# Kernel optimization log

Hardware: AMD Instinct MI355X
Metric: run time of the kernel (lower is better)

Reference implementation:

```python
import jax, jax.numpy as jnp
from jax import lax
import numpy as np

N_HOS, N_TYPES, N_STRUCTS = 4, 16, 512
N_COMBOS = N_HOS * N_TYPES  # 64
HID = 1024
N_ITERS = 60  # fixed PDHG iterations (differentiable unrolled solver)


def setup_inputs() -> dict:
    key = jax.random.key(0)
    ks = jax.random.split(key, 8)
    X = jax.random.uniform(ks[0], (2048, N_HOS, N_TYPES), dtype=jnp.float32)
    # sparse 0/1 structure matrix; guarantee each structure touches >=1 combo
    S = (jax.random.uniform(ks[1], (N_COMBOS, N_STRUCTS)) < 0.08).astype(jnp.float32)
    cols = jnp.arange(N_STRUCTS)
    S = S.at[cols % N_COMBOS, cols].set(1.0)
    # MLP params (He-ish init)
    W1 = jax.random.normal(ks[2], (N_COMBOS, HID), dtype=jnp.float32) * (2.0 / N_COMBOS) ** 0.5
    b1 = jnp.zeros((HID,), jnp.float32)
    W2 = jax.random.normal(ks[3], (HID, HID), dtype=jnp.float32) * (2.0 / HID) ** 0.5
    b2 = jnp.zeros((HID,), jnp.float32)
    W3 = jax.random.normal(ks[4], (HID, N_STRUCTS), dtype=jnp.float32) * (2.0 / HID) ** 0.5
    b3 = jnp.zeros((N_STRUCTS,), jnp.float32)
    return {"X": X, "W1": W1, "b1": b1, "W2": W2, "b2": b2,
            "W3": W3, "b3": b3, "S": S, "batch_size": 2048}


def nn_forward(X, W1, b1, W2, b2, W3, b3):
    # torch loop applies act_fun after EVERY layer, including the last
    Z = X.reshape(X.shape[0], -1)                 # [B, n_hos*n_types]
    Z = jax.nn.relu(Z @ W1 + b1)
    Z = jax.nn.relu(Z @ W2 + b2)
    Z = jax.nn.relu(Z @ W3 + b3)                  # [B, n_structures]
    return Z


def solve_lp(S, W, B, Z, n_iters=N_ITERS):
    """Batched solve of: max_x W.x - ||x - Z||_2  s.t. x >= 0, S x <= B.
    PDHG (Chambolle-Pock) on  min_x f(x) + i{Kx <= c},
    f(x) = -W.x + ||x - Z||_2,  K = [S; -I],  c = [B; 0].
    Same optimization problem as the CvxpyLayer, solved by a fixed-iteration
    batched primal-dual method (differentiable via unrolling)."""
    batch, n = Z.shape
    m = S.shape[0]

    # ||K||_2 via power iteration on K^T K = S^T S + I (constant wrt params)
    def pow_step(v, _):
        v2 = S.T @ (S @ v) + v
        return v2 / jnp.linalg.norm(v2), None
    v0 = jnp.full((n,), 1.0 / np.sqrt(n), Z.dtype)
    v, _ = lax.scan(pow_step, v0, None, length=30)
    L = jnp.sqrt(jnp.vdot(v, S.T @ (S @ v) + v))
    L = lax.stop_gradient(L)
    tau = 0.9 / L
    sigma = 0.9 / L

    c = jnp.concatenate([B, jnp.zeros_like(Z)], axis=-1)  # [B, m+n]

    def Kx(x):
        return jnp.concatenate([x @ S.T, -x], axis=-1)    # [B, m+n]

    def KTy(y):
        return y[:, :m] @ S - y[:, m:]                    # [B, n]

    def prox_f(v):
        # argmin_x 1/(2 tau) ||x - v||^2 - W.x + ||x - Z||_2
        u = v + tau * W
        d = u - Z
        nrm = jnp.linalg.norm(d, axis=-1, keepdims=True)
        scale = jnp.maximum(1.0 - tau / jnp.maximum(nrm, 1e-12), 0.0)
        return Z + scale * d

    def step(carry, _):
        x, xbar, y = carry
        y = jnp.maximum(y + sigma * (Kx(xbar) - c), 0.0)
        x_new = prox_f(x - tau * KTy(y))
        xbar = 2.0 * x_new - x
        return (x_new, xbar, y), None

    x0 = jnp.zeros_like(Z)
    y0 = jnp.zeros((batch, m + n), Z.dtype)
    (x, _, _), _ = lax.scan(step, (x0, x0, y0), None, length=n_iters)
    return x


def reference(X, W1, b1, W2, b2, W3, b3, S, batch_size):
    Z = nn_forward(X, W1, b1, W2, b2, W3, b3)     # [B, n_structures]
    W = jnp.ones_like(Z)                          # weights w = 1 (as in torch)
    B = X.reshape(batch_size, -1)                 # capacities b
    return solve_lp(S, W, B, Z)
```

## Files before the change

### kernel.cpp

```cpp
#include <hip/hip_runtime.h>


typedef _Float16 half8 __attribute__((ext_vector_type(8)));
typedef __fp16 fp16x2 __attribute__((ext_vector_type(2)));
typedef __fp16 fp16x4 __attribute__((ext_vector_type(4)));
typedef float floatx4 __attribute__((ext_vector_type(4)));

#define BATCH 2048
#define NITERS 60
#define XBS 520
#define YLS 72
#define H1S 1032

template <int CTRL>
__device__ __forceinline__ float dpp_addf(float x) {
    int y = __builtin_amdgcn_update_dpp(0, __builtin_bit_cast(int, x), CTRL, 0xf, 0xf, true);
    return x + __builtin_bit_cast(float, y);
}
__device__ __forceinline__ float sum16(float x) {
    x = dpp_addf<0xB1>(x);
    x = dpp_addf<0x4E>(x);
    x = dpp_addf<0x124>(x);
    x = dpp_addf<0x128>(x);
    return x;
}
__device__ __forceinline__ float sum64(float x) {
    x = sum16(x);
    x += __builtin_bit_cast(float, __builtin_amdgcn_ds_swizzle(__builtin_bit_cast(int, x), 0x401F));
    x += __shfl_xor(x, 32, 64);
    return x;
}

__device__ void power_64(const float* __restrict__ S, float* __restrict__ tau_g) {
    __shared__ unsigned long long rowm[64][8];
    __shared__ float G[64][65];
    __shared__ float wl[64], pg[4][64];
    int t = threadIdx.x, wv = t >> 6, ln = t & 63;
    for (int rr = 0; rr < 16; rr++) {
        int r = wv * 16 + rr;
        float v[8];
#pragma unroll
        for (int e = 0; e < 8; e++) v[e] = S[r * 512 + e * 64 + ln];
#pragma unroll
        for (int e = 0; e < 8; e++) {
            unsigned long long m = __ballot(v[e] != 0.f);
            if (ln == 0) rowm[r][e] = m;
        }
    }
    __syncthreads();
    for (int k = 0; k < 16; k++) {
        int idx = t * 16 + k;
        int i = idx >> 6, j = idx & 63;
        int cnt = 0;
#pragma unroll
        for (int e = 0; e < 8; e++) cnt += __popcll(rowm[i][e] & rowm[j][e]);
        G[i][j] = (float)cnt;
    }
    if (wv == 0) {
        int cnt = 0;
#pragma unroll
        for (int e = 0; e < 8; e++) cnt += __popcll(rowm[ln][e]);
        wl[ln] = (float)cnt * 0.044194173824159216f;
    }
    __syncthreads();
    for (int s = 0; s < 30; s++) {
        float a = 0.f;
#pragma unroll
        for (int jj = 0; jj < 16; jj++) {
            int j = wv * 16 + jj;
            a += G[ln][j] * wl[j];
        }
        pg[wv][ln] = a;
        __syncthreads();
        if (wv == 0) {
            float g = (pg[0][ln] + pg[1][ln]) + (pg[2][ln] + pg[3][ln]);
            float wi = wl[ln];
            float s1 = sum64(wi * g);
            float s2 = sum64(wi * wi);
            float n = sqrtf(s1 + 2.f * s2 + 1.f);
            wl[ln] = (g + wi) / n;
        }
        __syncthreads();
    }
    if (wv == 0) {
        float wi = wl[ln];
        float s2 = sum64(wi * wi);
        if (ln == 0) tau_g[0] = 0.9f / sqrtf(s2 + 1.f);
    }
}

__global__ __launch_bounds__(256) void prep(
    const float* __restrict__ W1, _Float16* __restrict__ w1f,
    const float* __restrict__ W2, _Float16* __restrict__ w2f,
    const float* __restrict__ W3, _Float16* __restrict__ w3f,
    const float* __restrict__ S, _Float16* __restrict__ s1f,
    _Float16* __restrict__ s2f, float* __restrict__ tau_g) {
    int tid = threadIdx.x;
    int bid = blockIdx.x;
    if (bid < 32) {
        int i0 = (bid * 256 + tid) * 8;
        int lane = (i0 >> 3) & 63, cf = (i0 >> 9) & 63, kk = i0 >> 15;
        int col = (cf >> 4) * 256 + (cf & 15) * 16 + (lane & 15);
        int kb = kk * 32 + ((lane >> 4) << 3);
        half8 vv;
#pragma unroll
        for (int j = 0; j < 8; j++)
            vv[j] = (_Float16)W1[(size_t)(kb + j) * 1024 + col];
        *(half8*)&w1f[i0] = vv;
        return;
    }
    if (bid < 544) {
        int i0 = ((bid - 32) * 256 + tid) * 8;
        int lane = (i0 >> 3) & 63, cf = (i0 >> 9) & 63, ks = i0 >> 15;
        int col = (cf >> 4) * 256 + (cf & 15) * 16 + (lane & 15);
        int kb = ks * 32 + ((lane >> 4) << 3);
        half8 vv;
#pragma unroll
        for (int j = 0; j < 8; j++)
            vv[j] = (_Float16)W2[(size_t)(kb + j) * 1024 + col];
        *(half8*)&w2f[i0] = vv;
        return;
    }
    if (bid < 800) {
        int i0 = ((bid - 544) * 256 + tid) * 8;
        int lane = (i0 >> 3) & 63, cf = (i0 >> 9) & 31, ks = i0 >> 14;
        int col = (cf >> 3) * 128 + (cf & 7) * 16 + (lane & 15);
        int kb = ks * 32 + ((lane >> 4) << 3);
        half8 vv;
#pragma unroll
        for (int j = 0; j < 8; j++)
            vv[j] = (_Float16)W3[(size_t)(kb + j) * 512 + col];
        *(half8*)&w3f[i0] = vv;
        return;
    }
    if (bid < 1056) {
        int i = (bid - 800) * 256 + tid;
        if (i < 4 * 16 * 64 * 8) {
            int j = i & 7, lane = (i >> 3) & 63, kk = (i >> 9) & 15, wc = i >> 13;
            int pos = kk * 32 + (lane >> 4) * 8 + j;
            int pp = pos >> 7, r = pos & 127;
            int hh = r >> 6, r2 = r & 63;
            int lmc = r2 >> 2, t3 = r2 & 3;
            int c = pp * 128 + (hh * 4 + t3) * 16 + lmc;
            int m = wc * 16 + (lane & 15);
            s1f[i] = (_Float16)S[m * 512 + c];
        } else {
            int i2 = i - 4 * 16 * 64 * 8;
            int j = i2 & 7, lane = (i2 >> 3) & 63, c = (i2 >> 9) & 1,
                tt = (i2 >> 10) & 7, wc = i2 >> 13;
            int kc = c * 32 + (lane >> 4) * 8 + j;
            int n = wc * 128 + tt * 16 + (lane & 15);
            s2f[i2] = (_Float16)S[kc * 512 + n];
        }
        return;
    }
    power_64(S, tau_g);
}

__global__ __launch_bounds__(256, 1) void mega(
    const float* __restrict__ X,
    const _Float16* __restrict__ w1f, const float* __restrict__ b1,
    const _Float16* __restrict__ w2f, const float* __restrict__ b2,
    const _Float16* __restrict__ w3f, const float* __restrict__ b3,
    const _Float16* __restrict__ s1f, const _Float16* __restrict__ s2f,
    const float* __restrict__ tau_p, float* __restrict__ out) {
    __shared__ __align__(16) char smem[34304];
    _Float16* H1 = (_Float16*)smem;
    _Float16* H2 = (_Float16*)(smem + 16512);
    _Float16* X8 = (_Float16*)(smem + 33024);
    _Float16* xb_d = (_Float16*)smem;
    _Float16* yl_d = (_Float16*)(smem + 8320);
    float (*red)[4] = (float(*)[4])(smem + 9472);

    int tid = threadIdx.x;
    int wp = tid >> 6;
    int l = tid & 63, lm = l & 15, q = l >> 4;
    int lq = lm & 7;
    int qa = q & 1, h = q >> 1;
    int b0 = blockIdx.x * 8;

    if (tid < 128) {
        int r = tid >> 4, c = (tid & 15) * 4;
        floatx4 v = *(const floatx4*)&X[(size_t)(b0 + r) * 64 + c];
        fp16x4 hh = {(__fp16)v.x, (__fp16)v.y, (__fp16)v.z, (__fp16)v.w};
        *(fp16x4*)&X8[r * 72 + c] = hh;
    }
    __syncthreads();

    {
        floatx4 acc1[16] = {};
#pragma unroll
        for (int kk = 0; kk < 2; kk++) {
            half8 a = *(const half8*)&X8[lq * 72 + kk * 32 + q * 8];
#pragma unroll
            for (int u = 0; u < 16; u++) {
                half8 b = *(const half8*)&w1f[((kk * 64 + wp * 16 + u) * 64 + l) * 8];
                acc1[u] = __builtin_amdgcn_mfma_f32_16x16x32_f16(a, b, acc1[u], 0, 0, 0);
            }
        }
        if (q < 2) {
#pragma unroll
            for (int u = 0; u < 16; u++) {
                int col = wp * 256 + u * 16 + lm;
                float bv = b1[col];
#pragma unroll
                for (int v = 0; v < 4; v++)
                    H1[(q * 4 + v) * H1S + col] = (_Float16)fmaxf(acc1[u][v] + bv, 0.f);
            }
        }
    }
    __syncthreads();

    {
        floatx4 acc2h[16] = {};
        half8 B2[16];
#pragma unroll
        for (int u = 0; u < 16; u++)
            B2[u] = *(const half8*)&w2f[((0 * 64 + wp * 16 + u) * 64 + l) * 8];
        half8 a_cur = *(const half8*)&H1[lq * H1S + q * 8];
#pragma unroll 1
        for (int ks = 0; ks < 32; ks++) {
            int ksn = (ks + 1) & 31;
            half8 a_nxt = *(const half8*)&H1[lq * H1S + ksn * 32 + q * 8];
#pragma unroll
            for (int u = 0; u < 16; u++) {
                half8 bn = *(const half8*)&w2f[((ksn * 64 + wp * 16 + u) * 64 + l) * 8];
                acc2h[u] = __builtin_amdgcn_mfma_f32_16x16x32_f16(a_cur, B2[u], acc2h[u], 0, 0, 0);
                B2[u] = bn;
            }
            a_cur = a_nxt;
        }
        __syncthreads();
        if (q < 2) {
#pragma unroll
            for (int u = 0; u < 16; u++) {
                int col = wp * 256 + u * 16 + lm;
                float bv = b2[col];
#pragma unroll
                for (int v = 0; v < 4; v++)
                    H2[(q * 4 + v) * H1S + col] = (_Float16)fmaxf(acc2h[u][v] + bv, 0.f);
            }
        }
    }
    __syncthreads();

    floatx4 acc3[8] = {};
    {
        half8 B3[8];
#pragma unroll
        for (int u = 0; u < 8; u++)
            B3[u] = *(const half8*)&w3f[((0 * 32 + wp * 8 + u) * 64 + l) * 8];
        half8 a_cur = *(const half8*)&H2[lq * H1S + q * 8];
#pragma unroll 1
        for (int ks = 0; ks < 32; ks++) {
            int ksn = (ks + 1) & 31;
            half8 a_nxt = *(const half8*)&H2[lq * H1S + ksn * 32 + q * 8];
#pragma unroll
            for (int u = 0; u < 8; u++) {
                half8 bn = *(const half8*)&w3f[((ksn * 32 + wp * 8 + u) * 64 + l) * 8];
                acc3[u] = __builtin_amdgcn_mfma_f32_16x16x32_f16(a_cur, B3[u], acc3[u], 0, 0, 0);
                B3[u] = bn;
            }
            a_cur = a_nxt;
        }
    }
    __syncthreads();

    half8 s1[16], s2[8][2];
#pragma unroll
    for (int k = 0; k < 16; k++)
        s1[k] = *(const half8*)&s1f[((wp * 16 + k) * 64 + l) * 8];
#pragma unroll
    for (int u = 0; u < 8; u++)
#pragma unroll
        for (int c = 0; c < 2; c++)
            s2[u][c] = *(const half8*)&s2f[(((wp * 8 + u) * 2 + c) * 64 + l) * 8];

    floatx4 z4[4], tz4[4], x4[4], xb4[4], yh4[4], d4[4];
    floatx4 ylo = {}, Bc;
    floatx4 a1p[4] = {};
    floatx4 acc2[8] = {};
    const floatx4 zero4 = {0.f, 0.f, 0.f, 0.f};
    float tau = tau_p[0];
    float sig = tau;

#pragma unroll
    for (int v = 0; v < 4; v++)
        Bc[v] = X[(size_t)(b0 + qa * 4 + v) * 64 + wp * 16 + lm];
#pragma unroll
    for (int t = 0; t < 4; t++) {
        int col = wp * 128 + (h * 4 + t) * 16 + lm;
        float bv = b3[col];
#pragma unroll
        for (int v = 0; v < 4; v++) {
            float zz = fmaxf(acc3[h * 4 + t][v] + bv, 0.f);
            z4[t][v] = zz;
            tz4[t][v] = tau - zz;
        }
        x4[t] = zero4; xb4[t] = zero4; yh4[t] = zero4;
    }
    {
        half8 hz = {0, 0, 0, 0, 0, 0, 0, 0};
        for (int i = tid; i < (8 * XBS) / 8; i += 256)
            *(half8*)&xb_d[i * 8] = hz;
        for (int i = tid; i < 8 * YLS; i += 256)
            yl_d[i] = (_Float16)0.f;
    }
    __syncthreads();

#pragma unroll 1
    for (int it = 0; it < NITERS; ++it) {
#pragma unroll
        for (int k = 0; k < 16; k++) {
            half8 ad = *(const half8*)&xb_d[lq * XBS + k * 32 + q * 8];
            a1p[k & 3] = __builtin_amdgcn_mfma_f32_16x16x32_f16(ad, s1[k], a1p[k & 3], 0, 0, 0);
        }
        floatx4 a1 = (a1p[0] + a1p[1]) + (a1p[2] + a1p[3]);
        floatx4 yv = __builtin_elementwise_max(ylo + sig * (a1 - Bc), zero4);
        floatx4 dy = yv - ylo;
        ylo = yv;
        if (q < 2) {
#pragma unroll
            for (int v = 0; v < 4; v++)
                yl_d[(q * 4 + v) * YLS + wp * 16 + lm] = (_Float16)dy[v];
        }
        __syncthreads();
        half8 a2d[2];
#pragma unroll
        for (int c = 0; c < 2; c++)
            a2d[c] = *(const half8*)&yl_d[lq * YLS + c * 32 + q * 8];
#pragma unroll
        for (int u = 0; u < 8; u++)
#pragma unroll
            for (int c = 0; c < 2; c++)
                acc2[u] = __builtin_amdgcn_mfma_f32_16x16x32_f16(a2d[c], s2[u][c], acc2[u], 0, 0, 0);
        floatx4 pn = {};
#pragma unroll
        for (int t = 0; t < 4; t++) {
            floatx4 accs = h ? acc2[t + 4] : acc2[t];
            yh4[t] = __builtin_elementwise_max(yh4[t] - sig * xb4[t], zero4);
            floatx4 kty = accs - yh4[t];
            floatx4 dd = (x4[t] - tau * kty) + tz4[t];
            d4[t] = dd;
            pn += dd * dd;
        }
#pragma unroll
        for (int v = 0; v < 4; v++) pn[v] = sum16(pn[v]);
#pragma unroll
        for (int v = 0; v < 4; v++) pn[v] += __shfl_xor(pn[v], 32, 64);
        if (lm == 0 && q < 2) {
#pragma unroll
            for (int v = 0; v < 4; v++) red[q * 4 + v][wp] = pn[v];
        }
        __syncthreads();
        floatx4 sv;
#pragma unroll
        for (int v = 0; v < 4; v++) {
            floatx4 rr = *(const floatx4*)&red[qa * 4 + v][0];
            float n2 = (rr.x + rr.y) + (rr.z + rr.w);
            sv[v] = fmaxf(1.f - tau * rsqrtf(fmaxf(n2, 1e-24f)), 0.f);
        }
#pragma unroll
        for (int t = 0; t < 4; t++) {
            floatx4 xn = z4[t] + sv * d4[t];
            floatx4 xbn = 2.f * xn - x4[t];
            d4[t] = xbn - xb4[t];
            x4[t] = xn;
            xb4[t] = xbn;
        }
#pragma unroll
        for (int v = 0; v < 4; v++) {
            fp16x2 p0 = __builtin_amdgcn_cvt_pkrtz(d4[0][v], d4[1][v]);
            fp16x2 p1 = __builtin_amdgcn_cvt_pkrtz(d4[2][v], d4[3][v]);
            fp16x4 hd = __builtin_shufflevector(p0, p1, 0, 1, 2, 3);
            *(fp16x4*)&xb_d[(qa * 4 + v) * XBS + wp * 128 + h * 64 + lm * 4] = hd;
        }
        __syncthreads();
    }
#pragma unroll
    for (int t = 0; t < 4; t++)
#pragma unroll
        for (int v = 0; v < 4; v++)
            out[(size_t)(b0 + qa * 4 + v) * 512 + wp * 128 + (h * 4 + t) * 16 + lm] = x4[t][v];
}

extern "C" void kernel_launch(void* const* d_in, const int* in_sizes, int n_in,
                              void* d_out, int out_size, void* d_ws, size_t ws_size,
                              hipStream_t stream) {
    const float* X  = (const float*)d_in[0];
    const float* W1 = (const float*)d_in[1];
    const float* b1 = (const float*)d_in[2];
    const float* W2 = (const float*)d_in[3];
    const float* b2 = (const float*)d_in[4];
    const float* W3 = (const float*)d_in[5];
    const float* b3 = (const float*)d_in[6];
    const float* S  = (const float*)d_in[7];
    float* out = (float*)d_out;

    char* ws = (char*)d_ws;
    size_t off = 0;
    auto alloc = [&](size_t bytes) {
        void* p = ws + off;
        off += (bytes + 255) & ~(size_t)255;
        return p;
    };
    _Float16* w1f = (_Float16*)alloc((size_t)65536 * 2);
    _Float16* w2f = (_Float16*)alloc((size_t)1048576 * 2);
    _Float16* w3f = (_Float16*)alloc((size_t)524288 * 2);
    _Float16* s1f = (_Float16*)alloc((size_t)4 * 16 * 64 * 8 * 2);
    _Float16* s2f = (_Float16*)alloc((size_t)4 * 8 * 2 * 64 * 8 * 2);
    float*    tau = (float*)alloc(256);

    hipLaunchKernelGGL(prep, dim3(1057), dim3(256), 0, stream,
                       W1, w1f, W2, w2f, W3, w3f, S, s1f, s2f, tau);
    hipLaunchKernelGGL(mega, dim3(BATCH / 8), dim3(256), 0, stream,
                       X, w1f, b1, w2f, b2, w3f, b3, s1f, s2f, tau, out);
}
```

Baseline: 233.3 us.

## Split fused mega kernel into separate 512-thread MLP and PDHG kernels

```diff
diff --git a/kernel.cpp b/kernel.cpp
--- a/kernel.cpp
+++ b/kernel.cpp
@@ -157,26 +157,19 @@
     power_64(S, tau_g);
 }
 
-__global__ __launch_bounds__(256, 1) void mega(
+__global__ __launch_bounds__(512) void mlp(
     const float* __restrict__ X,
     const _Float16* __restrict__ w1f, const float* __restrict__ b1,
     const _Float16* __restrict__ w2f, const float* __restrict__ b2,
     const _Float16* __restrict__ w3f, const float* __restrict__ b3,
-    const _Float16* __restrict__ s1f, const _Float16* __restrict__ s2f,
-    const float* __restrict__ tau_p, float* __restrict__ out) {
-    __shared__ __align__(16) char smem[34304];
-    _Float16* H1 = (_Float16*)smem;
-    _Float16* H2 = (_Float16*)(smem + 16512);
-    _Float16* X8 = (_Float16*)(smem + 33024);
-    _Float16* xb_d = (_Float16*)smem;
-    _Float16* yl_d = (_Float16*)(smem + 8320);
-    float (*red)[4] = (float(*)[4])(smem + 9472);
-
+    float* __restrict__ Zb) {
+    __shared__ __align__(16) _Float16 H1[8 * H1S];
+    __shared__ __align__(16) _Float16 H2[8 * H1S];
+    __shared__ __align__(16) _Float16 X8[8 * 72];
     int tid = threadIdx.x;
-    int wp = tid >> 6;
+    int w = tid >> 6;
     int l = tid & 63, lm = l & 15, q = l >> 4;
     int lq = lm & 7;
-    int qa = q & 1, h = q >> 1;
     int b0 = blockIdx.x * 8;
 
     if (tid < 128) {
@@ -188,20 +181,21 @@
     __syncthreads();
 
     {
-        floatx4 acc1[16] = {};
+        floatx4 acc1[8] = {};
 #pragma unroll
         for (int kk = 0; kk < 2; kk++) {
             half8 a = *(const half8*)&X8[lq * 72 + kk * 32 + q * 8];
 #pragma unroll
-            for (int u = 0; u < 16; u++) {
-                half8 b = *(const half8*)&w1f[((kk * 64 + wp * 16 + u) * 64 + l) * 8];
+            for (int u = 0; u < 8; u++) {
+                half8 b = *(const half8*)&w1f[((kk * 64 + w * 8 + u) * 64 + l) * 8];
                 acc1[u] = __builtin_amdgcn_mfma_f32_16x16x32_f16(a, b, acc1[u], 0, 0, 0);
             }
         }
         if (q < 2) {
 #pragma unroll
-            for (int u = 0; u < 16; u++) {
-                int col = wp * 256 + u * 16 + lm;
+            for (int u = 0; u < 8; u++) {
+                int cf = w * 8 + u;
+                int col = (cf >> 4) * 256 + (cf & 15) * 16 + lm;
                 float bv = b1[col];
 #pragma unroll
                 for (int v = 0; v < 4; v++)
@@ -212,20 +206,20 @@
     __syncthreads();
 
     {
-        floatx4 acc2h[16] = {};
-        half8 B2[16];
-#pragma unroll
-        for (int u = 0; u < 16; u++)
-            B2[u] = *(const half8*)&w2f[((0 * 64 + wp * 16 + u) * 64 + l) * 8];
+        floatx4 acc2[8] = {};
+        half8 B2[8];
+#pragma unroll
+        for (int u = 0; u < 8; u++)
+            B2[u] = *(const half8*)&w2f[((w * 8 + u) * 64 + l) * 8];
         half8 a_cur = *(const half8*)&H1[lq * H1S + q * 8];
 #pragma unroll 1
         for (int ks = 0; ks < 32; ks++) {
             int ksn = (ks + 1) & 31;
             half8 a_nxt = *(const half8*)&H1[lq * H1S + ksn * 32 + q * 8];
 #pragma unroll
-            for (int u = 0; u < 16; u++) {
-                half8 bn = *(const half8*)&w2f[((ksn * 64 + wp * 16 + u) * 64 + l) * 8];
-                acc2h[u] = __builtin_amdgcn_mfma_f32_16x16x32_f16(a_cur, B2[u], acc2h[u], 0, 0, 0);
+            for (int u = 0; u < 8; u++) {
+                half8 bn = *(const half8*)&w2f[((ksn * 64 + w * 8 + u) * 64 + l) * 8];
+                acc2[u] = __builtin_amdgcn_mfma_f32_16x16x32_f16(a_cur, B2[u], acc2[u], 0, 0, 0);
                 B2[u] = bn;
             }
             a_cur = a_nxt;
@@ -233,48 +227,75 @@
         __syncthreads();
         if (q < 2) {
 #pragma unroll
-            for (int u = 0; u < 16; u++) {
-                int col = wp * 256 + u * 16 + lm;
+            for (int u = 0; u < 8; u++) {
+                int cf = w * 8 + u;
+                int col = (cf >> 4) * 256 + (cf & 15) * 16 + lm;
                 float bv = b2[col];
 #pragma unroll
                 for (int v = 0; v < 4; v++)
-                    H2[(q * 4 + v) * H1S + col] = (_Float16)fmaxf(acc2h[u][v] + bv, 0.f);
-            }
-        }
-    }
-    __syncthreads();
-
-    floatx4 acc3[8] = {};
+                    H2[(q * 4 + v) * H1S + col] = (_Float16)fmaxf(acc2[u][v] + bv, 0.f);
+            }
+        }
+    }
+    __syncthreads();
+
     {
-        half8 B3[8];
-#pragma unroll
-        for (int u = 0; u < 8; u++)
-            B3[u] = *(const half8*)&w3f[((0 * 32 + wp * 8 + u) * 64 + l) * 8];
+        floatx4 acc3[4] = {};
+        half8 B3[4];
+#pragma unroll
+        for (int u = 0; u < 4; u++)
+            B3[u] = *(const half8*)&w3f[((w * 4 + u) * 64 + l) * 8];
         half8 a_cur = *(const half8*)&H2[lq * H1S + q * 8];
 #pragma unroll 1
         for (int ks = 0; ks < 32; ks++) {
             int ksn = (ks + 1) & 31;
             half8 a_nxt = *(const half8*)&H2[lq * H1S + ksn * 32 + q * 8];
 #pragma unroll
-            for (int u = 0; u < 8; u++) {
-                half8 bn = *(const half8*)&w3f[((ksn * 32 + wp * 8 + u) * 64 + l) * 8];
+            for (int u = 0; u < 4; u++) {
+                half8 bn = *(const half8*)&w3f[((ksn * 32 + w * 4 + u) * 64 + l) * 8];
                 acc3[u] = __builtin_amdgcn_mfma_f32_16x16x32_f16(a_cur, B3[u], acc3[u], 0, 0, 0);
                 B3[u] = bn;
             }
             a_cur = a_nxt;
         }
-    }
-    __syncthreads();
+        if (q < 2) {
+#pragma unroll
+            for (int u = 0; u < 4; u++) {
+                int cf = w * 4 + u;
+                int col = (cf >> 3) * 128 + (cf & 7) * 16 + lm;
+                float bv = b3[col];
+#pragma unroll
+                for (int v = 0; v < 4; v++)
+                    Zb[(size_t)(b0 + q * 4 + v) * 512 + col] = fmaxf(acc3[u][v] + bv, 0.f);
+            }
+        }
+    }
+}
+
+__global__ __launch_bounds__(256, 1) void pdhg_mfma(
+    const float* __restrict__ Zb, const float* __restrict__ Xf,
+    const _Float16* __restrict__ s1f, const _Float16* __restrict__ s2f,
+    const float* __restrict__ tau_p, float* __restrict__ out) {
+    __shared__ __align__(16) _Float16 xb_d[8 * XBS];
+    __shared__ __align__(16) _Float16 yl_d[8 * YLS];
+    __shared__ __align__(16) float red[8][4];
+    int tid = threadIdx.x;
+    int p = tid >> 6;
+    int l = tid & 63, lm = l & 15, q = l >> 4;
+    int lq = lm & 7;
+    int qa = q & 1;
+    int h = q >> 1;
+    int b0 = blockIdx.x * 8;
 
     half8 s1[16], s2[8][2];
 #pragma unroll
     for (int k = 0; k < 16; k++)
-        s1[k] = *(const half8*)&s1f[((wp * 16 + k) * 64 + l) * 8];
+        s1[k] = *(const half8*)&s1f[((p * 16 + k) * 64 + l) * 8];
 #pragma unroll
     for (int u = 0; u < 8; u++)
 #pragma unroll
         for (int c = 0; c < 2; c++)
-            s2[u][c] = *(const half8*)&s2f[(((wp * 8 + u) * 2 + c) * 64 + l) * 8];
+            s2[u][c] = *(const half8*)&s2f[(((p * 8 + u) * 2 + c) * 64 + l) * 8];
 
     floatx4 z4[4], tz4[4], x4[4], xb4[4], yh4[4], d4[4];
     floatx4 ylo = {}, Bc;
@@ -286,14 +307,12 @@
 
 #pragma unroll
     for (int v = 0; v < 4; v++)
-        Bc[v] = X[(size_t)(b0 + qa * 4 + v) * 64 + wp * 16 + lm];
+        Bc[v] = Xf[(b0 + qa * 4 + v) * 64 + p * 16 + lm];
 #pragma unroll
     for (int t = 0; t < 4; t++) {
-        int col = wp * 128 + (h * 4 + t) * 16 + lm;
-        float bv = b3[col];
 #pragma unroll
         for (int v = 0; v < 4; v++) {
-            float zz = fmaxf(acc3[h * 4 + t][v] + bv, 0.f);
+            float zz = Zb[(size_t)(b0 + qa * 4 + v) * 512 + p * 128 + (h * 4 + t) * 16 + lm];
             z4[t][v] = zz;
             tz4[t][v] = tau - zz;
         }
@@ -322,7 +341,7 @@
         if (q < 2) {
 #pragma unroll
             for (int v = 0; v < 4; v++)
-                yl_d[(q * 4 + v) * YLS + wp * 16 + lm] = (_Float16)dy[v];
+                yl_d[(q * 4 + v) * YLS + p * 16 + lm] = (_Float16)dy[v];
         }
         __syncthreads();
         half8 a2d[2];
@@ -350,7 +369,7 @@
         for (int v = 0; v < 4; v++) pn[v] += __shfl_xor(pn[v], 32, 64);
         if (lm == 0 && q < 2) {
 #pragma unroll
-            for (int v = 0; v < 4; v++) red[q * 4 + v][wp] = pn[v];
+            for (int v = 0; v < 4; v++) red[q * 4 + v][p] = pn[v];
         }
         __syncthreads();
         floatx4 sv;
@@ -373,7 +392,7 @@
             fp16x2 p0 = __builtin_amdgcn_cvt_pkrtz(d4[0][v], d4[1][v]);
             fp16x2 p1 = __builtin_amdgcn_cvt_pkrtz(d4[2][v], d4[3][v]);
             fp16x4 hd = __builtin_shufflevector(p0, p1, 0, 1, 2, 3);
-            *(fp16x4*)&xb_d[(qa * 4 + v) * XBS + wp * 128 + h * 64 + lm * 4] = hd;
+            *(fp16x4*)&xb_d[(qa * 4 + v) * XBS + p * 128 + h * 64 + lm * 4] = hd;
         }
         __syncthreads();
     }
@@ -381,7 +400,7 @@
     for (int t = 0; t < 4; t++)
 #pragma unroll
         for (int v = 0; v < 4; v++)
-            out[(size_t)(b0 + qa * 4 + v) * 512 + wp * 128 + (h * 4 + t) * 16 + lm] = x4[t][v];
+            out[(size_t)(b0 + qa * 4 + v) * 512 + p * 128 + (h * 4 + t) * 16 + lm] = x4[t][v];
 }
 
 extern "C" void kernel_launch(void* const* d_in, const int* in_sizes, int n_in,
@@ -410,9 +429,12 @@
     _Float16* s1f = (_Float16*)alloc((size_t)4 * 16 * 64 * 8 * 2);
     _Float16* s2f = (_Float16*)alloc((size_t)4 * 8 * 2 * 64 * 8 * 2);
     float*    tau = (float*)alloc(256);
+    float*    Zb  = (float*)alloc((size_t)BATCH * 512 * 4);
 
     hipLaunchKernelGGL(prep, dim3(1057), dim3(256), 0, stream,
                        W1, w1f, W2, w2f, W3, w3f, S, s1f, s2f, tau);
-    hipLaunchKernelGGL(mega, dim3(BATCH / 8), dim3(256), 0, stream,
-                       X, w1f, b1, w2f, b2, w3f, b3, s1f, s2f, tau, out);
-}
+    hipLaunchKernelGGL(mlp, dim3(BATCH / 8), dim3(512), 0, stream,
+                       X, w1f, b1, w2f, b2, w3f, b3, Zb);
+    hipLaunchKernelGGL(pdhg_mfma, dim3(BATCH / 8), dim3(256), 0, stream,
+                       Zb, X, s1f, s2f, tau, out);
+}
```

New measurement: 248.5 us. 1.06x slower.
